# Kernel optimization log

Measured on AMD Instinct MI355X. Metric: run time of the kernel, lower is better.

The kernel has to match this reference:

```python
import jax, jax.numpy as jnp
import numpy as np


def _mlp(x, ws, bs):
    # Linear->ReLU between layers, final Linear has no activation
    for i, (w, b) in enumerate(zip(ws, bs)):
        x = x @ w + b
        if i < len(ws) - 1:
            x = jax.nn.relu(x)
    return x


def setup_inputs() -> dict:
    key = jax.random.key(0)
    ks = jax.random.split(key, 24)
    n, q, H, W, dim = 2, 131072, 64, 2048, 64
    num = 4
    depth = jax.random.normal(ks[0], (n, 3, H, W), dtype=jnp.float32)
    feat = jax.random.normal(ks[1], (n, dim, H, W), dtype=jnp.float32)
    coord = jax.random.uniform(ks[2], (n, q, 2), dtype=jnp.float32, minval=-1.0, maxval=1.0)

    def lin(k, din, dout):
        kw, kb = jax.random.split(k)
        s = 1.0 / np.sqrt(din)
        w = jax.random.uniform(kw, (din, dout), minval=-s, maxval=s, dtype=jnp.float32)
        b = jax.random.uniform(kb, (dout,), minval=-s, maxval=s, dtype=jnp.float32)
        return w, b

    # pos_embedd: 2*num=8 -> [dim, num//2*dim] = [64,128] -> num*dim=256
    pe_dims = [2 * num, dim, (num // 2) * dim, num * dim]
    # encoder_xy: num*dim=256 -> [num*dim, num//2*dim, dim] = [256,128,64] -> num=4
    enc_dims = [num * dim, num * dim, (num // 2) * dim, dim, num]
    inp = {"depth": depth, "feat": feat, "coord": coord}
    for i in range(3):
        w, b = lin(ks[3 + i], pe_dims[i], pe_dims[i + 1])
        inp[f"pe_w{i}"] = w
        inp[f"pe_b{i}"] = b
    for i in range(4):
        w, b = lin(ks[8 + i], enc_dims[i], enc_dims[i + 1])
        inp[f"enc_w{i}"] = w
        inp[f"enc_b{i}"] = b
    return inp


def reference(depth, feat, coord,
              pe_w0, pe_b0, pe_w1, pe_b1, pe_w2, pe_b2,
              enc_w0, enc_b0, enc_w1, enc_b1, enc_w2, enc_b2, enc_w3, enc_b3):
    n, C, H, W = feat.shape
    q = coord.shape[1]
    eps = 1e-6
    # xy range-view magnitude map [n, H, W]
    xy = jnp.sqrt(depth[:, 1] ** 2 + depth[:, 2] ** 2)

    rx = 1.0 / H  # 2 / H / 2
    ry = 1.0 / W
    # offsets in the same (vx outer, vy inner) order as the torch loop
    offs = jnp.array([[-1.0, -1.0], [-1.0, 1.0], [1.0, -1.0], [1.0, 1.0]], dtype=coord.dtype)
    shift = offs * jnp.array([rx, ry], dtype=coord.dtype) + eps  # [4,2]
    c = jnp.clip(coord[None] + shift[:, None, None, :], -1.0 + 1e-6, 1.0 - 1e-6)  # [4,n,q,2]

    # nearest grid_sample, align_corners=False: unnormalized = ((g+1)*size - 1)/2, then round
    iy = jnp.clip(jnp.round(((c[..., 0] + 1.0) * H - 1.0) * 0.5).astype(jnp.int32), 0, H - 1)
    ix = jnp.clip(jnp.round(((c[..., 1] + 1.0) * W - 1.0) * 0.5).astype(jnp.int32), 0, W - 1)

    b = jnp.arange(n)[None, :, None]  # broadcasts against [4,n,q]
    q_feat = feat[b, :, iy, ix]      # [4,n,q,C] nearest-gathered features
    pred_xy = xy[b, iy, ix]          # [4,n,q]

    # sampled pixel-center coords (what grid_sample of feat_coord returns)
    qc_y = -1.0 + (2.0 * iy.astype(coord.dtype) + 1.0) / H
    qc_x = -1.0 + (2.0 * ix.astype(coord.dtype) + 1.0) / W
    rel = jnp.stack([(coord[None, ..., 0] - qc_y) * H,
                     (coord[None, ..., 1] - qc_x) * W], axis=-1)  # [4,n,q,2]

    # rearrange 't n q d -> (n q) (t d)'
    qf = q_feat.transpose(1, 2, 0, 3).reshape(n * q, 4 * C)
    rc = rel.transpose(1, 2, 0, 3).reshape(n * q, 4 * 2)

    qf = qf + _mlp(rc, [pe_w0, pe_w1, pe_w2], [pe_b0, pe_b1, pe_b2])
    logits = _mlp(qf, [enc_w0, enc_w1, enc_w2, enc_w3], [enc_b0, enc_b1, enc_b2, enc_b3])  # [nq,4]
    w = jax.nn.softmax(logits, axis=1)

    p = pred_xy.transpose(1, 2, 0).reshape(n * q, 4)  # 't n q -> (n q) t'
    ret = jnp.sum(p * w, axis=1).reshape(n, q, 1)     # [nq,1,4] @ [nq,4,1]
    return ret
```

## Files before the change

kernel.cpp:

```cpp
#include <hip/hip_runtime.h>
#include <hip/hip_runtime_api.h>
#include <math.h>

#define NBATCH 2
#define QQ     131072
#define HH     64
#define WWID   2048
#define CC     64
#define HWSZ   (HH*WWID)

constexpr int ROWS    = 64;
constexpr int THREADS = 256;

constexpr int ASTR_B = 512;

constexpr int OFF_A   = 0;
constexpr int OFF_TAP = 32768;
constexpr int OFF_PXY = OFF_TAP + 1024;
constexpr int OFF_E3  = OFF_PXY + 1024;
constexpr int LDS_BYTES = OFF_E3 + 1024;

constexpr int WOFF_PE0 = 0;
constexpr int WOFF_PE1 = 4096;
constexpr int WOFF_PE2 = 12288;
constexpr int WOFF_E0  = 45056;
constexpr int WOFF_E1  = 110592;
constexpr int WOFF_E2  = 143360;
constexpr int WTOTAL   = 151552;

typedef __attribute__((ext_vector_type(8))) short bf16x8;
typedef __attribute__((ext_vector_type(4))) float f32x4;

__device__ __forceinline__ ushort f2bf(float f) {
    union { float f; unsigned u; } x; x.f = f;
    unsigned r = x.u + 0x7fffu + ((x.u >> 16) & 1u);
    return (ushort)(r >> 16);
}
__device__ __forceinline__ float bf2f(ushort h) {
    union { unsigned u; float f; } x; x.u = ((unsigned)h) << 16;
    return x.f;
}
__device__ __forceinline__ unsigned cvtpk(float a, float b) {
    unsigned r;
    asm("v_cvt_pk_bf16_f32 %0, %1, %2" : "=v"(r) : "v"(a), "v"(b));
    return r;
}

__device__ __forceinline__ int swA(int row, int colByte) {
    return row * ASTR_B + (colByte ^ ((row & 7) << 4));
}

struct WDesc { const float* src; int K; int N; int kshift; };
struct WPack { WDesc d[6]; };

__global__ __launch_bounds__(256) void prep_weights(WPack p, ushort* __restrict__ dst)
{
    int e = blockIdx.x * 256 + threadIdx.x;
    int off = 0;
    #pragma unroll
    for (int L = 0; L < 6; ++L) {
        const int Kp = 1 << p.d[L].kshift;
        const int N  = p.d[L].N;
        const int sz = N * Kp;
        if (e < sz) {
            const int n = e / Kp;
            const int k = e & (Kp - 1);
            const float v = (k < p.d[L].K) ? p.d[L].src[(size_t)k * N + n] : 0.f;
            const int chunk = k >> 6;
            const int kk    = (k >> 5) & 1;
            const int tile  = chunk * ((N >> 4) * 2) + (n >> 4) * 2 + kk;
            const int lane  = (n & 15) + (((k >> 3) & 3) << 4);
            const int j     = k & 7;
            dst[off + tile * 512 + lane * 8 + j] = f2bf(v);
            return;
        }
        e -= sz; off += sz;
    }
}

__global__ __launch_bounds__(256) void prep_feat(
    const float* __restrict__ depth, const float* __restrict__ feat,
    ushort* __restrict__ nhwc, float* __restrict__ xy)
{
    const int idx = blockIdx.x * 256 + threadIdx.x;
    const int b   = idx >> 17;
    const int yx  = idx & (HWSZ - 1);

    const float d1 = depth[(b * 3 + 1) * HWSZ + yx];
    const float d2 = depth[(b * 3 + 2) * HWSZ + yx];
    xy[idx] = sqrtf(d1 * d1 + d2 * d2);

    const float* fp = feat + (size_t)b * CC * HWSZ + yx;
    ushort* op = nhwc + (size_t)idx * CC;
    #pragma unroll
    for (int c = 0; c < CC; c += 8) {
        union { uint4 v; ushort u[8]; } t;
        #pragma unroll
        for (int j = 0; j < 8; ++j) t.u[j] = f2bf(fp[(size_t)(c + j) * HWSZ]);
        *(uint4*)(op + c) = t.v;
    }
}

template <int K, int N, bool RELU>
__device__ __forceinline__ void dense_layer(
    char* __restrict__ sA, const ushort* __restrict__ Wt,
    const float* __restrict__ Bg, int tid)
{
    constexpr int TN  = N / 64;
    constexpr int NCH = K / 64;

    const int lane = tid & 63, wv = tid >> 6;
    const int col0 = wv * (N / 4);
    const int lrow = lane & 15;
    const int lkb  = (lane >> 4) * 16;

    f32x4 acc[4][TN];
    #pragma unroll
    for (int tm = 0; tm < 4; ++tm)
        #pragma unroll
        for (int tn = 0; tn < TN; ++tn) acc[tm][tn] = (f32x4){0.f, 0.f, 0.f, 0.f};

    const char* wbase = (const char*)Wt + (size_t)lane * 16;

    for (int c = 0; c < NCH; ++c) {
        #pragma unroll
        for (int ks = 0; ks < 64; ks += 32) {
            const int cb = (c * 64 + ks) * 2 + lkb;
            const bf16x8 a0 = *(const bf16x8*)(sA + swA(     lrow, cb));
            const bf16x8 a1 = *(const bf16x8*)(sA + swA(16 + lrow, cb));
            const bf16x8 a2 = *(const bf16x8*)(sA + swA(32 + lrow, cb));
            const bf16x8 a3 = *(const bf16x8*)(sA + swA(48 + lrow, cb));
            #pragma unroll
            for (int tn = 0; tn < TN; ++tn) {
                const int tile = c * ((N >> 4) * 2) + ((col0 >> 4) + tn) * 2 + (ks >> 5);
                const bf16x8 bw = *(const bf16x8*)(wbase + tile * 1024);
                acc[0][tn] = __builtin_amdgcn_mfma_f32_16x16x32_bf16(bw, a0, acc[0][tn], 0, 0, 0);
                acc[1][tn] = __builtin_amdgcn_mfma_f32_16x16x32_bf16(bw, a1, acc[1][tn], 0, 0, 0);
                acc[2][tn] = __builtin_amdgcn_mfma_f32_16x16x32_bf16(bw, a2, acc[2][tn], 0, 0, 0);
                acc[3][tn] = __builtin_amdgcn_mfma_f32_16x16x32_bf16(bw, a3, acc[3][tn], 0, 0, 0);
            }
        }
    }
    __syncthreads();

    #pragma unroll
    for (int tn = 0; tn < TN; ++tn) {
        const int colb = col0 + tn * 16 + (lane >> 4) * 4;
        const float4 b4 = *(const float4*)(Bg + colb);
        #pragma unroll
        for (int tm = 0; tm < 4; ++tm) {
            float v0 = acc[tm][tn][0] + b4.x;
            float v1 = acc[tm][tn][1] + b4.y;
            float v2 = acc[tm][tn][2] + b4.z;
            float v3 = acc[tm][tn][3] + b4.w;
            if (RELU) {
                v0 = fmaxf(v0, 0.f); v1 = fmaxf(v1, 0.f);
                v2 = fmaxf(v2, 0.f); v3 = fmaxf(v3, 0.f);
            }
            uint2 pk;
            pk.x = cvtpk(v0, v1);
            pk.y = cvtpk(v2, v3);
            const int row = tm * 16 + lrow;
            *(uint2*)(sA + swA(row, colb * 2)) = pk;
        }
    }
    __syncthreads();
}

template <bool USE_WS>
__global__ __launch_bounds__(256, 3) void fused_kernel(
    const float* __restrict__ depth, const float* __restrict__ feat,
    const float* __restrict__ coord,
    const float* __restrict__ pb0, const float* __restrict__ pb1,
    const float* __restrict__ pb2,
    const float* __restrict__ eb0, const float* __restrict__ eb1,
    const float* __restrict__ eb2,
    const float* __restrict__ ew3, const float* __restrict__ eb3,
    const ushort* __restrict__ wt,
    const ushort* __restrict__ nhwc, const float* __restrict__ xyws,
    float* __restrict__ out)
{
    extern __shared__ char lds[];
    char*  sA   = lds + OFF_A;
    int*   sTap = (int*)(lds + OFF_TAP);
    float* sPxy = (float*)(lds + OFF_PXY);
    float* sE3  = (float*)(lds + OFF_E3);

    const int tid  = threadIdx.x;
    const int row0g = blockIdx.x * ROWS;
    const int b     = row0g >> 17;

    sE3[tid] = ew3[tid];

    {
        const int r = tid >> 2, q = tid & 3;
        uint4 z; z.x = z.y = z.z = z.w = 0u;
        *(uint4*)(sA + r * ASTR_B + q * 32)      = z;
        *(uint4*)(sA + r * ASTR_B + q * 32 + 16) = z;
    }
    __syncthreads();

    {
        #pragma clang fp contract(off)
        const int r = tid >> 2, s = tid & 3;
        const int row = row0g + r;
        const float cy = coord[row * 2 + 0];
        const float cx = coord[row * 2 + 1];
        const float offy = (s < 2) ? -1.f : 1.f;
        const float offx = (s & 1) ? 1.f : -1.f;
        const float rx = 1.f / (float)HH, ry = 1.f / (float)WWID;
        float ccy = cy + (offy * rx + 1e-6f);
        float ccx = cx + (offx * ry + 1e-6f);
        ccy = fminf(fmaxf(ccy, -1.f + 1e-6f), 1.f - 1e-6f);
        ccx = fminf(fmaxf(ccx, -1.f + 1e-6f), 1.f - 1e-6f);
        int iy = (int)rintf(((ccy + 1.f) * (float)HH - 1.f) * 0.5f);
        int ix = (int)rintf(((ccx + 1.f) * (float)WWID - 1.f) * 0.5f);
        iy = min(max(iy, 0), HH - 1);
        ix = min(max(ix, 0), WWID - 1);
        const float qcy = -1.f + (2.f * (float)iy + 1.f) / (float)HH;
        const float qcx = -1.f + (2.f * (float)ix + 1.f) / (float)WWID;
        *(ushort*)(sA + swA(r, s * 4 + 0)) = f2bf((cy - qcy) * (float)HH);
        *(ushort*)(sA + swA(r, s * 4 + 2)) = f2bf((cx - qcx) * (float)WWID);
        const int tap = iy * WWID + ix;
        sTap[r * 4 + s] = tap;
        float px;
        if (USE_WS) {
            px = xyws[b * HWSZ + tap];
        } else {
            const float d1 = depth[(b * 3 + 1) * HWSZ + tap];
            const float d2 = depth[(b * 3 + 2) * HWSZ + tap];
            px = sqrtf(d1 * d1 + d2 * d2);
        }
        sPxy[r * 4 + s] = px;
    }
    __syncthreads();

    dense_layer<64,  64,  true >(sA, wt + WOFF_PE0, pb0, tid);
    dense_layer<64,  128, true >(sA, wt + WOFF_PE1, pb1, tid);
    dense_layer<128, 256, false>(sA, wt + WOFF_PE2, pb2, tid);

    {
        const int gr = tid >> 2, gs = tid & 3;
        const int tap = sTap[gr * 4 + gs];
        const int cb0 = gs * 128;
        if (USE_WS) {
            const ushort* src = nhwc + ((size_t)b * HWSZ + tap) * CC;
            #pragma unroll
            for (int g = 0; g < 8; ++g) {
                char* dp = sA + swA(gr, cb0 + g * 16);
                union { uint4 v; ushort u[8]; } a, d;
                a.v = *(const uint4*)(src + g * 8);
                d.v = *(uint4*)dp;
                float s0 = bf2f(a.u[0]) + bf2f(d.u[0]);
                float s1 = bf2f(a.u[1]) + bf2f(d.u[1]);
                float s2 = bf2f(a.u[2]) + bf2f(d.u[2]);
                float s3 = bf2f(a.u[3]) + bf2f(d.u[3]);
                float s4 = bf2f(a.u[4]) + bf2f(d.u[4]);
                float s5 = bf2f(a.u[5]) + bf2f(d.u[5]);
                float s6 = bf2f(a.u[6]) + bf2f(d.u[6]);
                float s7 = bf2f(a.u[7]) + bf2f(d.u[7]);
                uint4 o;
                o.x = cvtpk(s0, s1); o.y = cvtpk(s2, s3);
                o.z = cvtpk(s4, s5); o.w = cvtpk(s6, s7);
                *(uint4*)dp = o;
            }
        } else {
            const float* fp = feat + (size_t)b * CC * HWSZ + tap;
            #pragma unroll 8
            for (int c = 0; c < CC; ++c) {
                ushort* p = (ushort*)(sA + swA(gr, cb0 + c * 2));
                *p = f2bf(bf2f(*p) + fp[(size_t)c * HWSZ]);
            }
        }
    }
    __syncthreads();

    dense_layer<256, 256, true>(sA, wt + WOFF_E0, eb0, tid);
    dense_layer<256, 128, true>(sA, wt + WOFF_E1, eb1, tid);
    dense_layer<128, 64,  true>(sA, wt + WOFF_E2, eb2, tid);

    {
        const int fr = tid >> 2, sub = tid & 3;
        union { uint4 v; ushort u[8]; } h0, h1;
        h0.v = *(const uint4*)(sA + swA(fr, sub * 32));
        h1.v = *(const uint4*)(sA + swA(fr, sub * 32 + 16));
        float l0 = 0.f, l1 = 0.f, l2 = 0.f, l3 = 0.f;
        #pragma unroll
        for (int kk = 0; kk < 8; ++kk) {
            const float a = bf2f(h0.u[kk]);
            const float4 w = ((const float4*)sE3)[sub * 16 + kk];
            l0 = fmaf(a, w.x, l0);
            l1 = fmaf(a, w.y, l1);
            l2 = fmaf(a, w.z, l2);
            l3 = fmaf(a, w.w, l3);
        }
        #pragma unroll
        for (int kk = 0; kk < 8; ++kk) {
            const float a = bf2f(h1.u[kk]);
            const float4 w = ((const float4*)sE3)[sub * 16 + 8 + kk];
            l0 = fmaf(a, w.x, l0);
            l1 = fmaf(a, w.y, l1);
            l2 = fmaf(a, w.z, l2);
            l3 = fmaf(a, w.w, l3);
        }
        #pragma unroll
        for (int m = 1; m <= 2; m <<= 1) {
            l0 += __shfl_xor(l0, m);
            l1 += __shfl_xor(l1, m);
            l2 += __shfl_xor(l2, m);
            l3 += __shfl_xor(l3, m);
        }
        if (sub == 0) {
            l0 += eb3[0]; l1 += eb3[1]; l2 += eb3[2]; l3 += eb3[3];
            const float m  = fmaxf(fmaxf(l0, l1), fmaxf(l2, l3));
            const float e0 = expf(l0 - m), e1 = expf(l1 - m);
            const float e2 = expf(l2 - m), e3 = expf(l3 - m);
            const float inv = 1.f / (e0 + e1 + e2 + e3);
            const float o = (sPxy[fr * 4 + 0] * e0 + sPxy[fr * 4 + 1] * e1 +
                             sPxy[fr * 4 + 2] * e2 + sPxy[fr * 4 + 3] * e3) * inv;
            out[row0g + fr] = o;
        }
    }
}

extern "C" void kernel_launch(void* const* d_in, const int* in_sizes, int n_in,
                              void* d_out, int out_size, void* d_ws, size_t ws_size,
                              hipStream_t stream)
{
    const float* depth = (const float*)d_in[0];
    const float* feat  = (const float*)d_in[1];
    const float* coord = (const float*)d_in[2];
    const float* pw0 = (const float*)d_in[3],  *pb0 = (const float*)d_in[4];
    const float* pw1 = (const float*)d_in[5],  *pb1 = (const float*)d_in[6];
    const float* pw2 = (const float*)d_in[7],  *pb2 = (const float*)d_in[8];
    const float* ew0 = (const float*)d_in[9],  *eb0 = (const float*)d_in[10];
    const float* ew1 = (const float*)d_in[11], *eb1 = (const float*)d_in[12];
    const float* ew2 = (const float*)d_in[13], *eb2 = (const float*)d_in[14];
    const float* ew3 = (const float*)d_in[15], *eb3 = (const float*)d_in[16];
    float* out = (float*)d_out;

    const size_t nhwc_bytes = (size_t)NBATCH * HWSZ * CC * 2;
    const size_t xy_bytes   = (size_t)NBATCH * HWSZ * 4;
    const size_t wt_bytes   = (size_t)WTOTAL * 2;
    const bool use_ws = (ws_size >= nhwc_bytes + xy_bytes + wt_bytes);

    ushort* nhwc = (ushort*)d_ws;
    float*  xyws = (float*)((char*)d_ws + nhwc_bytes);
    ushort* wt   = use_ws ? (ushort*)((char*)d_ws + nhwc_bytes + xy_bytes)
                          : (ushort*)d_ws;

    WPack pack;
    pack.d[0] = { pw0, 8,   64,  6 };
    pack.d[1] = { pw1, 64,  128, 6 };
    pack.d[2] = { pw2, 128, 256, 7 };
    pack.d[3] = { ew0, 256, 256, 8 };
    pack.d[4] = { ew1, 256, 128, 8 };
    pack.d[5] = { ew2, 128, 64,  7 };
    prep_weights<<<WTOTAL / 256, 256, 0, stream>>>(pack, wt);

    const int nblocks = (NBATCH * QQ) / ROWS;

    if (use_ws) {
        prep_feat<<<(NBATCH * HWSZ) / 256, 256, 0, stream>>>(depth, feat, nhwc, xyws);
        fused_kernel<true><<<nblocks, THREADS, LDS_BYTES, stream>>>(
            depth, feat, coord, pb0, pb1, pb2, eb0, eb1, eb2, ew3, eb3,
            wt, nhwc, xyws, out);
    } else {
        fused_kernel<false><<<nblocks, THREADS, LDS_BYTES, stream>>>(
            depth, feat, coord, pb0, pb1, pb2, eb0, eb1, eb2, ew3, eb3,
            wt, nhwc, xyws, out);
    }
}
```

Before: 140.8 us.

## Switch dense layers to 32x32x16 MFMA tiles and shrink first-layer K padding

Rewrites the per-block MLP layers to use 32x32x16 bf16 MFMA instead of 16x16x32. The weight pre-pack layout and the LDS swizzle change to match. The first positional-embedding layer now pads K to 16 instead of 64, which drops wasted MFMA work and the full zero-fill of the activation tile. The larger tiles should cut LDS operand loads per FLOP, but each wave now carries bigger accumulators, which could hurt occupancy under the 3-block launch bound.

```diff
diff --git a/kernel.cpp b/kernel.cpp
--- a/kernel.cpp
+++ b/kernel.cpp
@@ -21,15 +21,15 @@
 constexpr int LDS_BYTES = OFF_E3 + 1024;
 
 constexpr int WOFF_PE0 = 0;
-constexpr int WOFF_PE1 = 4096;
-constexpr int WOFF_PE2 = 12288;
-constexpr int WOFF_E0  = 45056;
-constexpr int WOFF_E1  = 110592;
-constexpr int WOFF_E2  = 143360;
-constexpr int WTOTAL   = 151552;
-
-typedef __attribute__((ext_vector_type(8))) short bf16x8;
-typedef __attribute__((ext_vector_type(4))) float f32x4;
+constexpr int WOFF_PE1 = 1024;
+constexpr int WOFF_PE2 = 9216;
+constexpr int WOFF_E0  = 41984;
+constexpr int WOFF_E1  = 107520;
+constexpr int WOFF_E2  = 140288;
+constexpr int WTOTAL   = 148480;
+
+typedef __attribute__((ext_vector_type(8)))  short bf16x8;
+typedef __attribute__((ext_vector_type(16))) float f32x16;
 
 __device__ __forceinline__ ushort f2bf(float f) {
     union { float f; unsigned u; } x; x.f = f;
@@ -47,7 +47,7 @@
 }
 
 __device__ __forceinline__ int swA(int row, int colByte) {
-    return row * ASTR_B + (colByte ^ ((row & 7) << 4));
+    return row * ASTR_B + (colByte ^ ((row & 15) << 4));
 }
 
 struct WDesc { const float* src; int K; int N; int kshift; };
@@ -66,10 +66,9 @@
             const int n = e / Kp;
             const int k = e & (Kp - 1);
             const float v = (k < p.d[L].K) ? p.d[L].src[(size_t)k * N + n] : 0.f;
-            const int chunk = k >> 6;
-            const int kk    = (k >> 5) & 1;
-            const int tile  = chunk * ((N >> 4) * 2) + (n >> 4) * 2 + kk;
-            const int lane  = (n & 15) + (((k >> 3) & 3) << 4);
+            const int kstep = k >> 4;
+            const int tile  = kstep * (N >> 5) + (n >> 5);
+            const int lane  = (n & 31) | (((k >> 3) & 1) << 5);
             const int j     = k & 7;
             dst[off + tile * 512 + lane * 8 + j] = f2bf(v);
             return;
@@ -106,62 +105,65 @@
     char* __restrict__ sA, const ushort* __restrict__ Wt,
     const float* __restrict__ Bg, int tid)
 {
-    constexpr int TN  = N / 64;
-    constexpr int NCH = K / 64;
+    constexpr int CT = (N == 256) ? 2 : 1;
+    constexpr int RG = (N == 64) ? 1 : 2;
+    constexpr int KS = K / 16;
 
     const int lane = tid & 63, wv = tid >> 6;
-    const int col0 = wv * (N / 4);
-    const int lrow = lane & 15;
-    const int lkb  = (lane >> 4) * 16;
-
-    f32x4 acc[4][TN];
+    const int row0 = (N == 64) ? (wv >> 1) * 32 : 0;
+    const int col0 = (N == 64) ? (wv & 1) * 32 : wv * (N / 4);
+    const int lrow = lane & 31;
+    const int lkb  = (lane >> 5) * 16;
+
+    f32x16 acc[RG][CT];
     #pragma unroll
-    for (int tm = 0; tm < 4; ++tm)
-        #pragma unroll
-        for (int tn = 0; tn < TN; ++tn) acc[tm][tn] = (f32x4){0.f, 0.f, 0.f, 0.f};
+    for (int rg = 0; rg < RG; ++rg)
+        #pragma unroll
+        for (int ct = 0; ct < CT; ++ct)
+            #pragma unroll
+            for (int t = 0; t < 16; ++t) acc[rg][ct][t] = 0.f;
 
     const char* wbase = (const char*)Wt + (size_t)lane * 16;
 
-    for (int c = 0; c < NCH; ++c) {
-        #pragma unroll
-        for (int ks = 0; ks < 64; ks += 32) {
-            const int cb = (c * 64 + ks) * 2 + lkb;
-            const bf16x8 a0 = *(const bf16x8*)(sA + swA(     lrow, cb));
-            const bf16x8 a1 = *(const bf16x8*)(sA + swA(16 + lrow, cb));
-            const bf16x8 a2 = *(const bf16x8*)(sA + swA(32 + lrow, cb));
-            const bf16x8 a3 = *(const bf16x8*)(sA + swA(48 + lrow, cb));
+    for (int kst = 0; kst < KS; ++kst) {
+        const int cb = kst * 32 + lkb;
+        bf16x8 a[RG];
+        #pragma unroll
+        for (int rg = 0; rg < RG; ++rg)
+            a[rg] = *(const bf16x8*)(sA + swA(row0 + rg * 32 + lrow, cb));
+        #pragma unroll
+        for (int ct = 0; ct < CT; ++ct) {
+            const int tile = kst * (N >> 5) + (col0 >> 5) + ct;
+            const bf16x8 bw = *(const bf16x8*)(wbase + tile * 1024);
             #pragma unroll
-            for (int tn = 0; tn < TN; ++tn) {
-                const int tile = c * ((N >> 4) * 2) + ((col0 >> 4) + tn) * 2 + (ks >> 5);
-                const bf16x8 bw = *(const bf16x8*)(wbase + tile * 1024);
-                acc[0][tn] = __builtin_amdgcn_mfma_f32_16x16x32_bf16(bw, a0, acc[0][tn], 0, 0, 0);
-                acc[1][tn] = __builtin_amdgcn_mfma_f32_16x16x32_bf16(bw, a1, acc[1][tn], 0, 0, 0);
-                acc[2][tn] = __builtin_amdgcn_mfma_f32_16x16x32_bf16(bw, a2, acc[2][tn], 0, 0, 0);
-                acc[3][tn] = __builtin_amdgcn_mfma_f32_16x16x32_bf16(bw, a3, acc[3][tn], 0, 0, 0);
+            for (int rg = 0; rg < RG; ++rg)
+                acc[rg][ct] = __builtin_amdgcn_mfma_f32_32x32x16_bf16(bw, a[rg], acc[rg][ct], 0, 0, 0);
+        }
+    }
+    __syncthreads();
+
+    #pragma unroll
+    for (int ct = 0; ct < CT; ++ct) {
+        #pragma unroll
+        for (int q = 0; q < 4; ++q) {
+            const int colb = col0 + ct * 32 + q * 8 + (lane >> 5) * 4;
+            const float4 b4 = *(const float4*)(Bg + colb);
+            #pragma unroll
+            for (int rg = 0; rg < RG; ++rg) {
+                float v0 = acc[rg][ct][q * 4 + 0] + b4.x;
+                float v1 = acc[rg][ct][q * 4 + 1] + b4.y;
+                float v2 = acc[rg][ct][q * 4 + 2] + b4.z;
+                float v3 = acc[rg][ct][q * 4 + 3] + b4.w;
+                if (RELU) {
+                    v0 = fmaxf(v0, 0.f); v1 = fmaxf(v1, 0.f);
+                    v2 = fmaxf(v2, 0.f); v3 = fmaxf(v3, 0.f);
+                }
+                uint2 pk;
+                pk.x = cvtpk(v0, v1);
+                pk.y = cvtpk(v2, v3);
+                const int row = row0 + rg * 32 + lrow;
+                *(uint2*)(sA + swA(row, colb * 2)) = pk;
             }
-        }
-    }
-    __syncthreads();
-
-    #pragma unroll
-    for (int tn = 0; tn < TN; ++tn) {
-        const int colb = col0 + tn * 16 + (lane >> 4) * 4;
-        const float4 b4 = *(const float4*)(Bg + colb);
-        #pragma unroll
-        for (int tm = 0; tm < 4; ++tm) {
-            float v0 = acc[tm][tn][0] + b4.x;
-            float v1 = acc[tm][tn][1] + b4.y;
-            float v2 = acc[tm][tn][2] + b4.z;
-            float v3 = acc[tm][tn][3] + b4.w;
-            if (RELU) {
-                v0 = fmaxf(v0, 0.f); v1 = fmaxf(v1, 0.f);
-                v2 = fmaxf(v2, 0.f); v3 = fmaxf(v3, 0.f);
-            }
-            uint2 pk;
-            pk.x = cvtpk(v0, v1);
-            pk.y = cvtpk(v2, v3);
-            const int row = tm * 16 + lrow;
-            *(uint2*)(sA + swA(row, colb * 2)) = pk;
         }
     }
     __syncthreads();
@@ -191,14 +193,6 @@
     const int b     = row0g >> 17;
 
     sE3[tid] = ew3[tid];
-
-    {
-        const int r = tid >> 2, q = tid & 3;
-        uint4 z; z.x = z.y = z.z = z.w = 0u;
-        *(uint4*)(sA + r * ASTR_B + q * 32)      = z;
-        *(uint4*)(sA + r * ASTR_B + q * 32 + 16) = z;
-    }
-    __syncthreads();
 
     {
         #pragma clang fp contract(off)
@@ -221,6 +215,10 @@
         const float qcx = -1.f + (2.f * (float)ix + 1.f) / (float)WWID;
         *(ushort*)(sA + swA(r, s * 4 + 0)) = f2bf((cy - qcy) * (float)HH);
         *(ushort*)(sA + swA(r, s * 4 + 2)) = f2bf((cx - qcx) * (float)WWID);
+        if (s == 0) {
+            uint4 z; z.x = z.y = z.z = z.w = 0u;
+            *(uint4*)(sA + swA(r, 16)) = z;
+        }
         const int tap = iy * WWID + ix;
         sTap[r * 4 + s] = tap;
         float px;
@@ -235,7 +233,7 @@
     }
     __syncthreads();
 
-    dense_layer<64,  64,  true >(sA, wt + WOFF_PE0, pb0, tid);
+    dense_layer<16,  64,  true >(sA, wt + WOFF_PE0, pb0, tid);
     dense_layer<64,  128, true >(sA, wt + WOFF_PE1, pb1, tid);
     dense_layer<128, 256, false>(sA, wt + WOFF_PE2, pb2, tid);
 
@@ -350,7 +348,7 @@
                           : (ushort*)d_ws;
 
     WPack pack;
-    pack.d[0] = { pw0, 8,   64,  6 };
+    pack.d[0] = { pw0, 8,   64,  4 };
     pack.d[1] = { pw1, 64,  128, 6 };
     pack.d[2] = { pw2, 128, 256, 7 };
     pack.d[3] = { ew0, 256, 256, 8 };
```

Result: no change. 139.7 us (-0.8%).
